# Optimization experiments

Hardware: AMD Instinct MI355X
Metric: run time of the kernel (lower is better)

The kernel has to match this reference:

```python
import jax, jax.numpy as jnp
import numpy as np

DIM = 1024


def setup_inputs() -> dict:
    key = jax.random.key(0)
    ks = jax.random.split(key, 10)
    B, SQ, SKV, D = 4, 2048, 2048, DIM
    s = 1.0 / np.sqrt(D)
    return {
        "query": jax.random.normal(ks[0], (B, SQ, D), dtype=jnp.float32),
        "key_value": jax.random.normal(ks[1], (B, SKV, D), dtype=jnp.float32),
        "Wq": jax.random.normal(ks[2], (D, D), dtype=jnp.float32) * s,
        "bq": jnp.zeros((D,), dtype=jnp.float32),
        "Wk": jax.random.normal(ks[3], (D, D), dtype=jnp.float32) * s,
        "bk": jnp.zeros((D,), dtype=jnp.float32),
        "Wv": jax.random.normal(ks[4], (D, D), dtype=jnp.float32) * s,
        "bv": jnp.zeros((D,), dtype=jnp.float32),
        "Wo": jax.random.normal(ks[5], (D, D), dtype=jnp.float32) * s,
        "bo": jnp.zeros((D,), dtype=jnp.float32),
    }


def reference(query, key_value, Wq, bq, Wk, bk, Wv, bv, Wo, bo):
    # Faithful to the Keras layer: NO 1/sqrt(d) scaling, single head.
    Q = jnp.einsum("bsd,de->bse", query, Wq) + bq            # [B,Sq,D]
    K = jnp.einsum("btd,de->bte", key_value, Wk) + bk        # [B,Skv,D]
    V = jnp.einsum("btd,de->bte", key_value, Wv) + bv        # [B,Skv,D]
    scores = jnp.einsum("bse,bte->bst", Q, K)                # [B,Sq,Skv]
    attn = jax.nn.softmax(scores, axis=-1)
    ctx = jnp.einsum("bst,bte->bse", attn, V)                # [B,Sq,D]
    return jnp.einsum("bse,ef->bsf", ctx, Wo) + bo
```

## Files before the change

kernel.cpp:

```cpp
#include <hip/hip_runtime.h>
#include <cstdint>

typedef unsigned short u16;
typedef _Float16 f16;
typedef __attribute__((ext_vector_type(8))) short    s8v;
typedef __attribute__((ext_vector_type(8))) _Float16 h8v;
typedef __attribute__((ext_vector_type(4))) float    f4v;

__device__ __forceinline__ float bf2f(u16 b) {
  unsigned int u = ((unsigned int)b) << 16;
  float f;
  __builtin_memcpy(&f, &u, 4);
  return f;
}
__device__ __forceinline__ u16 f2bf(float f) {
  unsigned int u;
  __builtin_memcpy(&u, &f, 4);
  u += 0x7fffu + ((u >> 16) & 1u);
  return (u16)(u >> 16);
}

__device__ __forceinline__ void glds16(const void* g, void* l) {
  __builtin_amdgcn_global_load_lds(
      (const __attribute__((address_space(1))) unsigned int*)g,
      (__attribute__((address_space(3))) unsigned int*)l, 16, 0, 0);
}

#define BM 128
#define BN 128
#define BK 32

__global__ __launch_bounds__(256)
void detect_dtype(const u16* __restrict__ q, int* __restrict__ flg)
{
  __shared__ int cbig, czero;
  if (threadIdx.x == 0) { cbig = 0; czero = 0; }
  __syncthreads();
  int b = 0, z = 0;
  for (int i = threadIdx.x; i < 4096; i += 256) {
    float v = bf2f(q[i]);
    if (!(fabsf(v) < 1e4f)) b++;
    if ((i & 1) == 0 && q[i] == 0) z++;
  }
  atomicAdd(&cbig, b);
  atomicAdd(&czero, z);
  __syncthreads();
  if (threadIdx.x == 0) flg[0] = (cbig > 64 || czero > 1600) ? 1 : 0;
}

__global__ __launch_bounds__(256)
void convert_h(const int* __restrict__ flg,
               const void* __restrict__ q, const void* __restrict__ kv,
               f16* __restrict__ qo, f16* __restrict__ kvo, long n)
{
  const void* in = blockIdx.y ? kv : q;
  f16* out = blockIdx.y ? kvo : qo;
  const long i = ((long)blockIdx.x * 256 + threadIdx.x) * 8;
  if (i >= n) return;
  h8v h;
  if (flg[0] != 0) {
    const float* p = (const float*)in + i;
    f4v f0 = *(const f4v*)p;
    f4v f1 = *(const f4v*)(p + 4);
#pragma unroll
    for (int j = 0; j < 4; ++j) {
      h[j]     = (f16)f0[j];
      h[4 + j] = (f16)f1[j];
    }
  } else {
    s8v b = *(const s8v*)((const short*)in + i);
#pragma unroll
    for (int j = 0; j < 8; ++j) h[j] = (f16)bf2f((u16)b[j]);
  }
  *(h8v*)(out + i) = h;
}

__global__ __launch_bounds__(256)
void transpose_w4(const int* __restrict__ flg,
                  const void* __restrict__ w0, const void* __restrict__ w1,
                  const void* __restrict__ w2, const void* __restrict__ w3,
                  f16* __restrict__ h0, f16* __restrict__ h1,
                  f16* __restrict__ h2, u16* __restrict__ b3, int D)
{
  __shared__ float tile[32][33];
  const int zb = blockIdx.z;
  const void* in_v = (zb == 0) ? w0 : (zb == 1) ? w1 : (zb == 2) ? w2 : w3;
  const bool i32 = (flg[0] != 0);
  const u16*   in16 = (const u16*)in_v;
  const float* in32 = (const float*)in_v;
  const int c0 = blockIdx.x * 32, r0 = blockIdx.y * 32;
  const int tx = threadIdx.x, ty = threadIdx.y;
  for (int i = ty; i < 32; i += 8) {
    const long idx = (long)(r0 + i) * D + c0 + tx;
    tile[i][tx] = i32 ? in32[idx] : bf2f(in16[idx]);
  }
  __syncthreads();
  f16* outH = (zb == 0) ? h0 : (zb == 1) ? h1 : h2;
  for (int i = ty; i < 32; i += 8) {
    const long idx = (long)(c0 + i) * D + r0 + tx;
    const float v = tile[tx][i];
    if (zb == 3) b3[idx]   = f2bf(v);
    else         outH[idx] = (f16)v;
  }
}

__global__ __launch_bounds__(256)
void gemm_proj_qk(const int* __restrict__ flg,
                  const f16* __restrict__ A0, const f16* __restrict__ B0,
                  const void* __restrict__ bias0, f16* __restrict__ o0,
                  const f16* __restrict__ A1, const f16* __restrict__ B1,
                  const void* __restrict__ bias1, f16* __restrict__ o1,
                  int M, int N, int K)
{
  __shared__ u16 As[BM * BK];
  __shared__ u16 Bs[BN * BK];

  const int zb = blockIdx.z;
  const f16* A = zb ? A1 : A0;
  const f16* B = zb ? B1 : B0;
  const void* bias = zb ? bias1 : bias0;
  f16* out = zb ? o1 : o0;

  const int f_in = flg[0];
  const int tid = threadIdx.x, lane = tid & 63, wave = tid >> 6;
  const int wm = wave >> 1, wn = wave & 1;
  const int m0 = blockIdx.y * BM, n0 = blockIdx.x * BN;

  const int rr  = wave * 32 + (lane >> 2);
  const int cc8 = (lane & 3) * 8;
  const f16* ga0 = A + (long)(m0 + rr) * K + cc8;
  const f16* ga1 = ga0 + 16 * (long)K;
  const f16* gb0 = B + (long)(n0 + rr) * K + cc8;
  const f16* gb1 = gb0 + 16 * (long)K;
  u16* la0 = &As[(wave * 2    ) * 512];
  u16* la1 = &As[(wave * 2 + 1) * 512];
  u16* lb0 = &Bs[(wave * 2    ) * 512];
  u16* lb1 = &Bs[(wave * 2 + 1) * 512];

  f4v acc[4][4];
#pragma unroll
  for (int i = 0; i < 4; ++i)
#pragma unroll
    for (int j = 0; j < 4; ++j) acc[i][j] = (f4v){0.f, 0.f, 0.f, 0.f};

  const int fr = lane & 15, fk = (lane >> 4) * 8;
  const int aoff = (wm * 64 + fr) * BK + fk;
  const int boff = (wn * 64 + fr) * BK + fk;

  for (int kt = 0; kt < K; kt += BK) {
    glds16(ga0, la0); glds16(ga1, la1);
    glds16(gb0, lb0); glds16(gb1, lb1);
    ga0 += BK; ga1 += BK; gb0 += BK; gb1 += BK;
    __syncthreads();

    h8v af[4], bfr[4];
#pragma unroll
    for (int mi = 0; mi < 4; ++mi) af[mi]  = *(const h8v*)&As[aoff + mi * 16 * BK];
#pragma unroll
    for (int ni = 0; ni < 4; ++ni) bfr[ni] = *(const h8v*)&Bs[boff + ni * 16 * BK];
#pragma unroll
    for (int mi = 0; mi < 4; ++mi)
#pragma unroll
      for (int ni = 0; ni < 4; ++ni)
        acc[mi][ni] = __builtin_amdgcn_mfma_f32_16x16x32_f16(af[mi], bfr[ni], acc[mi][ni], 0, 0, 0);
    __syncthreads();
  }

  const int cr = (lane >> 4) * 4, ccl = lane & 15;
#pragma unroll
  for (int ni = 0; ni < 4; ++ni) {
    const int gcol = n0 + wn * 64 + ni * 16 + ccl;
    const float bv = (f_in != 0) ? ((const float*)bias)[gcol]
                                 : bf2f(((const u16*)bias)[gcol]);
#pragma unroll
    for (int mi = 0; mi < 4; ++mi)
#pragma unroll
      for (int r = 0; r < 4; ++r) {
        const long grow = (long)(m0 + wm * 64 + mi * 16 + cr + r);
        out[grow * N + gcol] = (f16)(acc[mi][ni][r] + bv);
      }
  }
}

__global__ __launch_bounds__(256)
void gemm_vt(const int* __restrict__ flg, const f16* __restrict__ A,
             const f16* __restrict__ B, const void* __restrict__ bias,
             u16* __restrict__ Vt, int M, int N, int K, int SB)
{
  __shared__ u16 As[BM * BK];
  __shared__ u16 Bs[BN * BK];
  __shared__ u16 xp[4][64 * 34];

  const int f_in = flg[0];
  const int tid = threadIdx.x, lane = tid & 63, wave = tid >> 6;
  const int wm = wave >> 1, wn = wave & 1;
  const int m0 = blockIdx.y * BM, n0 = blockIdx.x * BN;

  const int rr  = wave * 32 + (lane >> 2);
  const int cc8 = (lane & 3) * 8;
  const f16* ga0 = A + (long)(m0 + rr) * K + cc8;
  const f16* ga1 = ga0 + 16 * (long)K;
  const f16* gb0 = B + (long)(n0 + rr) * K + cc8;
  const f16* gb1 = gb0 + 16 * (long)K;
  u16* la0 = &As[(wave * 2    ) * 512];
  u16* la1 = &As[(wave * 2 + 1) * 512];
  u16* lb0 = &Bs[(wave * 2    ) * 512];
  u16* lb1 = &Bs[(wave * 2 + 1) * 512];

  f4v acc[4][4];
#pragma unroll
  for (int i = 0; i < 4; ++i)
#pragma unroll
    for (int j = 0; j < 4; ++j) acc[i][j] = (f4v){0.f, 0.f, 0.f, 0.f};

  const int fr = lane & 15, fk = (lane >> 4) * 8;
  const int aoff = (wm * 64 + fr) * BK + fk;
  const int boff = (wn * 64 + fr) * BK + fk;

  for (int kt = 0; kt < K; kt += BK) {
    glds16(ga0, la0); glds16(ga1, la1);
    glds16(gb0, lb0); glds16(gb1, lb1);
    ga0 += BK; ga1 += BK; gb0 += BK; gb1 += BK;
    __syncthreads();

    h8v af[4], bfr[4];
#pragma unroll
    for (int mi = 0; mi < 4; ++mi) af[mi]  = *(const h8v*)&As[aoff + mi * 16 * BK];
#pragma unroll
    for (int ni = 0; ni < 4; ++ni) bfr[ni] = *(const h8v*)&Bs[boff + ni * 16 * BK];
#pragma unroll
    for (int mi = 0; mi < 4; ++mi)
#pragma unroll
      for (int ni = 0; ni < 4; ++ni)
        acc[mi][ni] = __builtin_amdgcn_mfma_f32_16x16x32_f16(af[mi], bfr[ni], acc[mi][ni], 0, 0, 0);
    __syncthreads();
  }

  const int cr = (lane >> 4) * 4, ccl = lane & 15;
  const int b  = m0 / SB;
  const int s0 = (m0 % SB) + wm * 64;
  u16* xw = &xp[wave][0];
  const long bbase = (long)b * N * SB;
#pragma unroll
  for (int h = 0; h < 2; ++h) {
#pragma unroll
    for (int nl = 0; nl < 2; ++nl) {
      const int ni = h * 2 + nl;
      const int gcol = n0 + wn * 64 + ni * 16 + ccl;
      const float bv = (f_in != 0) ? ((const float*)bias)[gcol]
                                   : bf2f(((const u16*)bias)[gcol]);
#pragma unroll
      for (int mi = 0; mi < 4; ++mi)
#pragma unroll
        for (int r = 0; r < 4; ++r)
          xw[(mi * 16 + cr + r) * 34 + nl * 16 + ccl] = f2bf(acc[mi][ni][r] + bv);
    }
    __syncthreads();
#pragma unroll
    for (int c = 0; c < 32; ++c) {
      const int gcol = n0 + wn * 64 + h * 32 + c;
      Vt[bbase + (long)gcol * SB + s0 + lane] = xw[lane * 34 + c];
    }
    __syncthreads();
  }
}

__global__ __launch_bounds__(256)
void gemm_sc(const f16* __restrict__ A, const f16* __restrict__ B,
             float* __restrict__ C, int M, int N, int K,
             long sA, long sB, long sC)
{
  __shared__ u16 As[BM * BK];
  __shared__ u16 Bs[BN * BK];

  const int tid = threadIdx.x, lane = tid & 63, wave = tid >> 6;
  const int wm = wave >> 1, wn = wave & 1;
  const int m0 = blockIdx.y * BM, n0 = blockIdx.x * BN;
  const long z = blockIdx.z;

  const int rr  = wave * 32 + (lane >> 2);
  const int cc8 = (lane & 3) * 8;
  const f16* ga0 = A + (long)(m0 + rr) * K + cc8 + z * sA;
  const f16* ga1 = ga0 + 16 * (long)K;
  const f16* gb0 = B + (long)(n0 + rr) * K + cc8 + z * sB;
  const f16* gb1 = gb0 + 16 * (long)K;
  u16* la0 = &As[(wave * 2    ) * 512];
  u16* la1 = &As[(wave * 2 + 1) * 512];
  u16* lb0 = &Bs[(wave * 2    ) * 512];
  u16* lb1 = &Bs[(wave * 2 + 1) * 512];

  f4v acc[4][4];
#pragma unroll
  for (int i = 0; i < 4; ++i)
#pragma unroll
    for (int j = 0; j < 4; ++j) acc[i][j] = (f4v){0.f, 0.f, 0.f, 0.f};

  const int fr = lane & 15, fk = (lane >> 4) * 8;
  const int aoff = (wm * 64 + fr) * BK + fk;
  const int boff = (wn * 64 + fr) * BK + fk;

  for (int kt = 0; kt < K; kt += BK) {
    glds16(ga0, la0); glds16(ga1, la1);
    glds16(gb0, lb0); glds16(gb1, lb1);
    ga0 += BK; ga1 += BK; gb0 += BK; gb1 += BK;
    __syncthreads();

    h8v af[4], bfr[4];
#pragma unroll
    for (int mi = 0; mi < 4; ++mi) af[mi]  = *(const h8v*)&As[aoff + mi * 16 * BK];
#pragma unroll
    for (int ni = 0; ni < 4; ++ni) bfr[ni] = *(const h8v*)&Bs[boff + ni * 16 * BK];
#pragma unroll
    for (int mi = 0; mi < 4; ++mi)
#pragma unroll
      for (int ni = 0; ni < 4; ++ni)
        acc[mi][ni] = __builtin_amdgcn_mfma_f32_16x16x32_f16(af[mi], bfr[ni], acc[mi][ni], 0, 0, 0);
    __syncthreads();
  }

  const int cr = (lane >> 4) * 4, ccl = lane & 15;
#pragma unroll
  for (int ni = 0; ni < 4; ++ni) {
    const int gcol = n0 + wn * 64 + ni * 16 + ccl;
#pragma unroll
    for (int mi = 0; mi < 4; ++mi)
#pragma unroll
      for (int r = 0; r < 4; ++r) {
        const long grow = (long)(m0 + wm * 64 + mi * 16 + cr + r);
        C[z * sC + grow * N + gcol] = acc[mi][ni][r];
      }
  }
}

template<bool OUT_FLAG, bool HAS_BIAS>
__global__ __launch_bounds__(256)
void gemm16(const int* __restrict__ flg, const u16* __restrict__ A,
            const u16* __restrict__ Bt, const void* __restrict__ bias,
            void* __restrict__ Cv, int M, int N, int K,
            long sA, long sB, long sC)
{
  __shared__ u16 As[BM * BK];
  __shared__ u16 Bs[BN * BK];

  const int f_in = flg[0];
  const int tid = threadIdx.x, lane = tid & 63, wave = tid >> 6;
  const int wm = wave >> 1, wn = wave & 1;
  const int m0 = blockIdx.y * BM, n0 = blockIdx.x * BN;
  const long z = blockIdx.z;
  const u16* Ap = A + z * sA;
  const u16* Bp = Bt + z * sB;

  const int rr  = wave * 32 + (lane >> 2);
  const int cc8 = (lane & 3) * 8;
  const u16* ga0 = Ap + (long)(m0 + rr) * K + cc8;
  const u16* ga1 = ga0 + 16 * (long)K;
  const u16* gb0 = Bp + (long)(n0 + rr) * K + cc8;
  const u16* gb1 = gb0 + 16 * (long)K;
  u16* la0 = &As[(wave * 2    ) * 512];
  u16* la1 = &As[(wave * 2 + 1) * 512];
  u16* lb0 = &Bs[(wave * 2    ) * 512];
  u16* lb1 = &Bs[(wave * 2 + 1) * 512];

  f4v acc[4][4];
#pragma unroll
  for (int i = 0; i < 4; ++i)
#pragma unroll
    for (int j = 0; j < 4; ++j) acc[i][j] = (f4v){0.f, 0.f, 0.f, 0.f};

  const int fr = lane & 15, fk = (lane >> 4) * 8;
  const int aoff = (wm * 64 + fr) * BK + fk;
  const int boff = (wn * 64 + fr) * BK + fk;

  for (int kt = 0; kt < K; kt += BK) {
    glds16(ga0, la0); glds16(ga1, la1);
    glds16(gb0, lb0); glds16(gb1, lb1);
    ga0 += BK; ga1 += BK; gb0 += BK; gb1 += BK;
    __syncthreads();

    s8v af[4], bfr[4];
#pragma unroll
    for (int mi = 0; mi < 4; ++mi) af[mi]  = *(const s8v*)&As[aoff + mi * 16 * BK];
#pragma unroll
    for (int ni = 0; ni < 4; ++ni) bfr[ni] = *(const s8v*)&Bs[boff + ni * 16 * BK];
#pragma unroll
    for (int mi = 0; mi < 4; ++mi)
#pragma unroll
      for (int ni = 0; ni < 4; ++ni)
        acc[mi][ni] = __builtin_amdgcn_mfma_f32_16x16x32_bf16(af[mi], bfr[ni], acc[mi][ni], 0, 0, 0);
    __syncthreads();
  }

  const int cr = (lane >> 4) * 4, ccl = lane & 15;
  const bool o32 = OUT_FLAG && (f_in != 0);
#pragma unroll
  for (int ni = 0; ni < 4; ++ni) {
    const int gcol = n0 + wn * 64 + ni * 16 + ccl;
    float bv = 0.f;
    if (HAS_BIAS)
      bv = (f_in != 0) ? ((const float*)bias)[gcol] : bf2f(((const u16*)bias)[gcol]);
#pragma unroll
    for (int mi = 0; mi < 4; ++mi)
#pragma unroll
      for (int r = 0; r < 4; ++r) {
        const long grow = (long)(m0 + wm * 64 + mi * 16 + cr + r);
        const float val = acc[mi][ni][r] + bv;
        const long idx = z * sC + grow * N + gcol;
        if (o32) ((float*)Cv)[idx] = val;
        else     ((u16*)Cv)[idx]   = f2bf(val);
      }
  }
}

__global__ __launch_bounds__(256)
void softmax_rows_bf(const float* __restrict__ S, u16* __restrict__ P, int N)
{
  const float* row = S + (long)blockIdx.x * N;
  u16* prow = P + (long)blockIdx.x * N;
  const int t = threadIdx.x;
  f4v v0 = *(const f4v*)(row + t * 8);
  f4v v1 = *(const f4v*)(row + t * 8 + 4);

  float m = v0[0];
#pragma unroll
  for (int j = 1; j < 4; ++j) m = fmaxf(m, v0[j]);
#pragma unroll
  for (int j = 0; j < 4; ++j) m = fmaxf(m, v1[j]);
  for (int off = 32; off > 0; off >>= 1) m = fmaxf(m, __shfl_down(m, off, 64));

  __shared__ float redm[4], reds[4];
  if ((t & 63) == 0) redm[t >> 6] = m;
  __syncthreads();
  m = fmaxf(fmaxf(redm[0], redm[1]), fmaxf(redm[2], redm[3]));

  float s = 0.f;
#pragma unroll
  for (int j = 0; j < 4; ++j) { v0[j] = __expf(v0[j] - m); s += v0[j]; }
#pragma unroll
  for (int j = 0; j < 4; ++j) { v1[j] = __expf(v1[j] - m); s += v1[j]; }
  for (int off = 32; off > 0; off >>= 1) s += __shfl_down(s, off, 64);
  if ((t & 63) == 0) reds[t >> 6] = s;
  __syncthreads();
  s = reds[0] + reds[1] + reds[2] + reds[3];

  const float inv = 1.f / s;
  s8v o;
#pragma unroll
  for (int j = 0; j < 4; ++j) {
    o[j]     = (short)f2bf(v0[j] * inv);
    o[4 + j] = (short)f2bf(v1[j] * inv);
  }
  *(s8v*)(prow + t * 8) = o;
}

extern "C" void kernel_launch(void* const* d_in, const int* in_sizes, int n_in,
                              void* d_out, int out_size, void* d_ws, size_t ws_size,
                              hipStream_t stream)
{
  const void* query = d_in[0];
  const void* kv    = d_in[1];
  const void* Wq    = d_in[2];
  const void* bq    = d_in[3];
  const void* Wk    = d_in[4];
  const void* bk    = d_in[5];
  const void* Wv    = d_in[6];
  const void* bv    = d_in[7];
  const void* Wo    = d_in[8];
  const void* bo    = d_in[9];

  const int Bn = 4, S = 2048, D = 1024;
  const int MS = Bn * S;
  const size_t KBu = 1024, MBu = 1024 * 1024;
  const long nTok = (long)MS * D;

  char* ws = (char*)d_ws;
  int*  flg  = (int*)(ws);
  f16*  Qi   = (f16*)(ws + 64 * KBu);
  f16*  KVi  = (f16*)(ws + 64 * KBu + 16 * MBu);
  char* rW   = ws + 64 * KBu + 32 * MBu;
  f16*  WqT  = (f16*)(rW);
  f16*  WkT  = (f16*)(rW + 2 * MBu);
  f16*  WvT  = (f16*)(rW + 4 * MBu);
  u16*  WoT  = (u16*)(rW + 6 * MBu);
  char* rQK  = rW + 8 * MBu;
  f16*  Qf   = (f16*)(rQK);
  f16*  Kf   = (f16*)(rQK + 16 * MBu);
  u16*  attn = (u16*)(rQK);
  float* Sc  = (float*)(rQK + 32 * MBu);
  char* rV   = rQK + 96 * MBu;
  u16*  Vt   = (u16*)(rV);
  u16*  Cx   = (u16*)(rV + 16 * MBu);

  detect_dtype<<<1, 256, 0, stream>>>((const u16*)query, flg);

  convert_h<<<dim3((unsigned)(nTok / 2048), 2), 256, 0, stream>>>(
      flg, query, kv, Qi, KVi, nTok);

  dim3 tb(32, 8);
  transpose_w4<<<dim3(32, 32, 4), tb, 0, stream>>>(
      flg, Wq, Wk, Wv, Wo, WqT, WkT, WvT, WoT, D);

  gemm_proj_qk<<<dim3(D / BN, MS / BM, 2), 256, 0, stream>>>(
      flg, Qi, WqT, bq, Qf, KVi, WkT, bk, Kf, MS, D, D);
  gemm_vt<<<dim3(D / BN, MS / BM, 1), 256, 0, stream>>>(
      flg, KVi, WvT, bv, Vt, MS, D, D, S);

  gemm_sc<<<dim3(S / BN, S / BM, Bn), 256, 0, stream>>>(
      Qf, Kf, Sc, S, S, D, (long)S * D, (long)S * D, (long)S * S);
  softmax_rows_bf<<<dim3(Bn * S), 256, 0, stream>>>(Sc, attn, S);
  gemm16<false, false><<<dim3(D / BN, S / BM, Bn), 256, 0, stream>>>(
      flg, attn, Vt, nullptr, Cx, S, D, S, (long)S * S, (long)D * S, (long)S * D);

  gemm16<true, true><<<dim3(D / BN, MS / BM, 1), 256, 0, stream>>>(
      flg, Cx, WoT, bo, d_out, MS, D, D, 0L, 0L, 0L);
}
```

Before: 417.0 us.

## Double GEMM K-step to 64 and merge Q/K/V projections into one launch

All GEMM kernels now load a 64-wide K slab per iteration, stored as two 32-wide halves in LDS. This halves the number of barrier pairs and load rounds per output tile. The Q, K and V projections are merged into a single three-slice launch, and the V-transpose epilogue reuses the operand LDS buffers as staging space. Shared memory per block doubles, which may lower occupancy.

```diff
diff --git a/kernel.cpp b/kernel.cpp
--- a/kernel.cpp
+++ b/kernel.cpp
@@ -28,7 +28,6 @@
 
 #define BM 128
 #define BN 128
-#define BK 32
 
 __global__ __launch_bounds__(256)
 void detect_dtype(const u16* __restrict__ q, int* __restrict__ flg)
@@ -105,21 +104,22 @@
 }
 
 __global__ __launch_bounds__(256)
-void gemm_proj_qk(const int* __restrict__ flg,
-                  const f16* __restrict__ A0, const f16* __restrict__ B0,
-                  const void* __restrict__ bias0, f16* __restrict__ o0,
-                  const f16* __restrict__ A1, const f16* __restrict__ B1,
-                  const void* __restrict__ bias1, f16* __restrict__ o1,
-                  int M, int N, int K)
-{
-  __shared__ u16 As[BM * BK];
-  __shared__ u16 Bs[BN * BK];
+void gemm_proj3(const int* __restrict__ flg,
+                const f16* __restrict__ Qi, const f16* __restrict__ KVi,
+                const f16* __restrict__ WqT, const f16* __restrict__ WkT,
+                const f16* __restrict__ WvT,
+                const void* __restrict__ bq, const void* __restrict__ bk,
+                const void* __restrict__ bv,
+                f16* __restrict__ Qf, f16* __restrict__ Kf,
+                u16* __restrict__ Vt, int M, int N, int K, int SB)
+{
+  __shared__ u16 As[BM * 64];
+  __shared__ u16 Bs[BN * 64];
 
   const int zb = blockIdx.z;
-  const f16* A = zb ? A1 : A0;
-  const f16* B = zb ? B1 : B0;
-  const void* bias = zb ? bias1 : bias0;
-  f16* out = zb ? o1 : o0;
+  const f16* A = (zb == 0) ? Qi : KVi;
+  const f16* B = (zb == 0) ? WqT : (zb == 1) ? WkT : WvT;
+  const void* bias = (zb == 0) ? bq : (zb == 1) ? bk : bv;
 
   const int f_in = flg[0];
   const int tid = threadIdx.x, lane = tid & 63, wave = tid >> 6;
@@ -128,14 +128,12 @@
 
   const int rr  = wave * 32 + (lane >> 2);
   const int cc8 = (lane & 3) * 8;
-  const f16* ga0 = A + (long)(m0 + rr) * K + cc8;
-  const f16* ga1 = ga0 + 16 * (long)K;
-  const f16* gb0 = B + (long)(n0 + rr) * K + cc8;
-  const f16* gb1 = gb0 + 16 * (long)K;
-  u16* la0 = &As[(wave * 2    ) * 512];
-  u16* la1 = &As[(wave * 2 + 1) * 512];
-  u16* lb0 = &Bs[(wave * 2    ) * 512];
-  u16* lb1 = &Bs[(wave * 2 + 1) * 512];
+  const f16* ga00 = A + (long)(m0 + rr) * K + cc8;
+  const f16* ga01 = ga00 + 16 * (long)K;
+  const f16* gb00 = B + (long)(n0 + rr) * K + cc8;
+  const f16* gb01 = gb00 + 16 * (long)K;
+  u16* la0 = &As[(wave * 2) * 512];  u16* la1 = la0 + 512;
+  u16* lb0 = &Bs[(wave * 2) * 512];  u16* lb1 = lb0 + 512;
 
   f4v acc[4][4];
 #pragma unroll
@@ -144,134 +142,97 @@
     for (int j = 0; j < 4; ++j) acc[i][j] = (f4v){0.f, 0.f, 0.f, 0.f};
 
   const int fr = lane & 15, fk = (lane >> 4) * 8;
-  const int aoff = (wm * 64 + fr) * BK + fk;
-  const int boff = (wn * 64 + fr) * BK + fk;
-
-  for (int kt = 0; kt < K; kt += BK) {
-    glds16(ga0, la0); glds16(ga1, la1);
-    glds16(gb0, lb0); glds16(gb1, lb1);
-    ga0 += BK; ga1 += BK; gb0 += BK; gb1 += BK;
+  const int aoff = (wm * 64 + fr) * 32 + fk;
+  const int boff = (wn * 64 + fr) * 32 + fk;
+
+  for (int kt = 0; kt < K; kt += 64) {
+    glds16(ga00,      la0);        glds16(ga01,      la1);
+    glds16(ga00 + 32, la0 + 4096); glds16(ga01 + 32, la1 + 4096);
+    glds16(gb00,      lb0);        glds16(gb01,      lb1);
+    glds16(gb00 + 32, lb0 + 4096); glds16(gb01 + 32, lb1 + 4096);
+    ga00 += 64; ga01 += 64; gb00 += 64; gb01 += 64;
     __syncthreads();
 
-    h8v af[4], bfr[4];
-#pragma unroll
-    for (int mi = 0; mi < 4; ++mi) af[mi]  = *(const h8v*)&As[aoff + mi * 16 * BK];
-#pragma unroll
-    for (int ni = 0; ni < 4; ++ni) bfr[ni] = *(const h8v*)&Bs[boff + ni * 16 * BK];
-#pragma unroll
-    for (int mi = 0; mi < 4; ++mi)
-#pragma unroll
-      for (int ni = 0; ni < 4; ++ni)
-        acc[mi][ni] = __builtin_amdgcn_mfma_f32_16x16x32_f16(af[mi], bfr[ni], acc[mi][ni], 0, 0, 0);
+    {
+      h8v af[4], bfr[4];
+#pragma unroll
+      for (int mi = 0; mi < 4; ++mi) af[mi]  = *(const h8v*)&As[aoff + mi * 512];
+#pragma unroll
+      for (int ni = 0; ni < 4; ++ni) bfr[ni] = *(const h8v*)&Bs[boff + ni * 512];
+#pragma unroll
+      for (int mi = 0; mi < 4; ++mi)
+#pragma unroll
+        for (int ni = 0; ni < 4; ++ni)
+          acc[mi][ni] = __builtin_amdgcn_mfma_f32_16x16x32_f16(af[mi], bfr[ni], acc[mi][ni], 0, 0, 0);
+    }
+    {
+      h8v af[4], bfr[4];
+#pragma unroll
+      for (int mi = 0; mi < 4; ++mi) af[mi]  = *(const h8v*)&As[4096 + aoff + mi * 512];
+#pragma unroll
+      for (int ni = 0; ni < 4; ++ni) bfr[ni] = *(const h8v*)&Bs[4096 + boff + ni * 512];
+#pragma unroll
+      for (int mi = 0; mi < 4; ++mi)
+#pragma unroll
+        for (int ni = 0; ni < 4; ++ni)
+          acc[mi][ni] = __builtin_amdgcn_mfma_f32_16x16x32_f16(af[mi], bfr[ni], acc[mi][ni], 0, 0, 0);
+    }
     __syncthreads();
   }
 
   const int cr = (lane >> 4) * 4, ccl = lane & 15;
-#pragma unroll
-  for (int ni = 0; ni < 4; ++ni) {
-    const int gcol = n0 + wn * 64 + ni * 16 + ccl;
-    const float bv = (f_in != 0) ? ((const float*)bias)[gcol]
-                                 : bf2f(((const u16*)bias)[gcol]);
-#pragma unroll
-    for (int mi = 0; mi < 4; ++mi)
-#pragma unroll
-      for (int r = 0; r < 4; ++r) {
-        const long grow = (long)(m0 + wm * 64 + mi * 16 + cr + r);
-        out[grow * N + gcol] = (f16)(acc[mi][ni][r] + bv);
+  if (zb < 2) {
+    f16* out = zb ? Kf : Qf;
+#pragma unroll
+    for (int ni = 0; ni < 4; ++ni) {
+      const int gcol = n0 + wn * 64 + ni * 16 + ccl;
+      const float bvv = (f_in != 0) ? ((const float*)bias)[gcol]
+                                    : bf2f(((const u16*)bias)[gcol]);
+#pragma unroll
+      for (int mi = 0; mi < 4; ++mi)
+#pragma unroll
+        for (int r = 0; r < 4; ++r) {
+          const long grow = (long)(m0 + wm * 64 + mi * 16 + cr + r);
+          out[grow * N + gcol] = (f16)(acc[mi][ni][r] + bvv);
+        }
+    }
+  } else {
+    u16* xw = (wave < 2) ? (&As[0] + wave * 2176) : (&Bs[0] + (wave - 2) * 2176);
+    const int b  = m0 / SB;
+    const int s0 = (m0 % SB) + wm * 64;
+    const long bbase = (long)b * N * SB;
+#pragma unroll
+    for (int h = 0; h < 2; ++h) {
+#pragma unroll
+      for (int nl = 0; nl < 2; ++nl) {
+        const int ni = h * 2 + nl;
+        const int gcol = n0 + wn * 64 + ni * 16 + ccl;
+        const float bvv = (f_in != 0) ? ((const float*)bias)[gcol]
+                                      : bf2f(((const u16*)bias)[gcol]);
+#pragma unroll
+        for (int mi = 0; mi < 4; ++mi)
+#pragma unroll
+          for (int r = 0; r < 4; ++r)
+            xw[(mi * 16 + cr + r) * 34 + nl * 16 + ccl] = f2bf(acc[mi][ni][r] + bvv);
       }
-  }
-}
-
-__global__ __launch_bounds__(256)
-void gemm_vt(const int* __restrict__ flg, const f16* __restrict__ A,
-             const f16* __restrict__ B, const void* __restrict__ bias,
-             u16* __restrict__ Vt, int M, int N, int K, int SB)
-{
-  __shared__ u16 As[BM * BK];
-  __shared__ u16 Bs[BN * BK];
-  __shared__ u16 xp[4][64 * 34];
-
-  const int f_in = flg[0];
-  const int tid = threadIdx.x, lane = tid & 63, wave = tid >> 6;
-  const int wm = wave >> 1, wn = wave & 1;
-  const int m0 = blockIdx.y * BM, n0 = blockIdx.x * BN;
-
-  const int rr  = wave * 32 + (lane >> 2);
-  const int cc8 = (lane & 3) * 8;
-  const f16* ga0 = A + (long)(m0 + rr) * K + cc8;
-  const f16* ga1 = ga0 + 16 * (long)K;
-  const f16* gb0 = B + (long)(n0 + rr) * K + cc8;
-  const f16* gb1 = gb0 + 16 * (long)K;
-  u16* la0 = &As[(wave * 2    ) * 512];
-  u16* la1 = &As[(wave * 2 + 1) * 512];
-  u16* lb0 = &Bs[(wave * 2    ) * 512];
-  u16* lb1 = &Bs[(wave * 2 + 1) * 512];
-
-  f4v acc[4][4];
-#pragma unroll
-  for (int i = 0; i < 4; ++i)
-#pragma unroll
-    for (int j = 0; j < 4; ++j) acc[i][j] = (f4v){0.f, 0.f, 0.f, 0.f};
-
-  const int fr = lane & 15, fk = (lane >> 4) * 8;
-  const int aoff = (wm * 64 + fr) * BK + fk;
-  const int boff = (wn * 64 + fr) * BK + fk;
-
-  for (int kt = 0; kt < K; kt += BK) {
-    glds16(ga0, la0); glds16(ga1, la1);
-    glds16(gb0, lb0); glds16(gb1, lb1);
-    ga0 += BK; ga1 += BK; gb0 += BK; gb1 += BK;
-    __syncthreads();
-
-    h8v af[4], bfr[4];
-#pragma unroll
-    for (int mi = 0; mi < 4; ++mi) af[mi]  = *(const h8v*)&As[aoff + mi * 16 * BK];
-#pragma unroll
-    for (int ni = 0; ni < 4; ++ni) bfr[ni] = *(const h8v*)&Bs[boff + ni * 16 * BK];
-#pragma unroll
-    for (int mi = 0; mi < 4; ++mi)
-#pragma unroll
-      for (int ni = 0; ni < 4; ++ni)
-        acc[mi][ni] = __builtin_amdgcn_mfma_f32_16x16x32_f16(af[mi], bfr[ni], acc[mi][ni], 0, 0, 0);
-    __syncthreads();
-  }
-
-  const int cr = (lane >> 4) * 4, ccl = lane & 15;
-  const int b  = m0 / SB;
-  const int s0 = (m0 % SB) + wm * 64;
-  u16* xw = &xp[wave][0];
-  const long bbase = (long)b * N * SB;
-#pragma unroll
-  for (int h = 0; h < 2; ++h) {
-#pragma unroll
-    for (int nl = 0; nl < 2; ++nl) {
-      const int ni = h * 2 + nl;
-      const int gcol = n0 + wn * 64 + ni * 16 + ccl;
-      const float bv = (f_in != 0) ? ((const float*)bias)[gcol]
-                                   : bf2f(((const u16*)bias)[gcol]);
-#pragma unroll
-      for (int mi = 0; mi < 4; ++mi)
-#pragma unroll
-        for (int r = 0; r < 4; ++r)
-          xw[(mi * 16 + cr + r) * 34 + nl * 16 + ccl] = f2bf(acc[mi][ni][r] + bv);
-    }
-    __syncthreads();
-#pragma unroll
-    for (int c = 0; c < 32; ++c) {
-      const int gcol = n0 + wn * 64 + h * 32 + c;
-      Vt[bbase + (long)gcol * SB + s0 + lane] = xw[lane * 34 + c];
-    }
-    __syncthreads();
-  }
-}
-
-__global__ __launch_bounds__(256)
-void gemm_sc(const f16* __restrict__ A, const f16* __restrict__ B,
-             float* __restrict__ C, int M, int N, int K,
-             long sA, long sB, long sC)
-{
-  __shared__ u16 As[BM * BK];
-  __shared__ u16 Bs[BN * BK];
+      __syncthreads();
+#pragma unroll
+      for (int c = 0; c < 32; ++c) {
+        const int gcol = n0 + wn * 64 + h * 32 + c;
+        Vt[bbase + (long)gcol * SB + s0 + lane] = xw[lane * 34 + c];
+      }
+      __syncthreads();
+    }
+  }
+}
+
+__global__ __launch_bounds__(256)
+void gemm_sc64(const f16* __restrict__ A, const f16* __restrict__ B,
+               float* __restrict__ C, int M, int N, int K,
+               long sA, long sB, long sC)
+{
+  __shared__ u16 As[BM * 64];
+  __shared__ u16 Bs[BN * 64];
 
   const int tid = threadIdx.x, lane = tid & 63, wave = tid >> 6;
   const int wm = wave >> 1, wn = wave & 1;
@@ -280,14 +241,12 @@
 
   const int rr  = wave * 32 + (lane >> 2);
   const int cc8 = (lane & 3) * 8;
-  const f16* ga0 = A + (long)(m0 + rr) * K + cc8 + z * sA;
-  const f16* ga1 = ga0 + 16 * (long)K;
-  const f16* gb0 = B + (long)(n0 + rr) * K + cc8 + z * sB;
-  const f16* gb1 = gb0 + 16 * (long)K;
-  u16* la0 = &As[(wave * 2    ) * 512];
-  u16* la1 = &As[(wave * 2 + 1) * 512];
-  u16* lb0 = &Bs[(wave * 2    ) * 512];
-  u16* lb1 = &Bs[(wave * 2 + 1) * 512];
+  const f16* ga00 = A + (long)(m0 + rr) * K + cc8 + z * sA;
+  const f16* ga01 = ga00 + 16 * (long)K;
+  const f16* gb00 = B + (long)(n0 + rr) * K + cc8 + z * sB;
+  const f16* gb01 = gb00 + 16 * (long)K;
+  u16* la0 = &As[(wave * 2) * 512];  u16* la1 = la0 + 512;
+  u16* lb0 = &Bs[(wave * 2) * 512];  u16* lb1 = lb0 + 512;
 
   f4v acc[4][4];
 #pragma unroll
@@ -296,25 +255,41 @@
     for (int j = 0; j < 4; ++j) acc[i][j] = (f4v){0.f, 0.f, 0.f, 0.f};
 
   const int fr = lane & 15, fk = (lane >> 4) * 8;
-  const int aoff = (wm * 64 + fr) * BK + fk;
-  const int boff = (wn * 64 + fr) * BK + fk;
-
-  for (int kt = 0; kt < K; kt += BK) {
-    glds16(ga0, la0); glds16(ga1, la1);
-    glds16(gb0, lb0); glds16(gb1, lb1);
-    ga0 += BK; ga1 += BK; gb0 += BK; gb1 += BK;
+  const int aoff = (wm * 64 + fr) * 32 + fk;
+  const int boff = (wn * 64 + fr) * 32 + fk;
+
+  for (int kt = 0; kt < K; kt += 64) {
+    glds16(ga00,      la0);        glds16(ga01,      la1);
+    glds16(ga00 + 32, la0 + 4096); glds16(ga01 + 32, la1 + 4096);
+    glds16(gb00,      lb0);        glds16(gb01,      lb1);
+    glds16(gb00 + 32, lb0 + 4096); glds16(gb01 + 32, lb1 + 4096);
+    ga00 += 64; ga01 += 64; gb00 += 64; gb01 += 64;
     __syncthreads();
 
-    h8v af[4], bfr[4];
-#pragma unroll
-    for (int mi = 0; mi < 4; ++mi) af[mi]  = *(const h8v*)&As[aoff + mi * 16 * BK];
-#pragma unroll
-    for (int ni = 0; ni < 4; ++ni) bfr[ni] = *(const h8v*)&Bs[boff + ni * 16 * BK];
-#pragma unroll
-    for (int mi = 0; mi < 4; ++mi)
-#pragma unroll
-      for (int ni = 0; ni < 4; ++ni)
-        acc[mi][ni] = __builtin_amdgcn_mfma_f32_16x16x32_f16(af[mi], bfr[ni], acc[mi][ni], 0, 0, 0);
+    {
+      h8v af[4], bfr[4];
+#pragma unroll
+      for (int mi = 0; mi < 4; ++mi) af[mi]  = *(const h8v*)&As[aoff + mi * 512];
+#pragma unroll
+      for (int ni = 0; ni < 4; ++ni) bfr[ni] = *(const h8v*)&Bs[boff + ni * 512];
+#pragma unroll
+      for (int mi = 0; mi < 4; ++mi)
+#pragma unroll
+        for (int ni = 0; ni < 4; ++ni)
+          acc[mi][ni] = __builtin_amdgcn_mfma_f32_16x16x32_f16(af[mi], bfr[ni], acc[mi][ni], 0, 0, 0);
+    }
+    {
+      h8v af[4], bfr[4];
+#pragma unroll
+      for (int mi = 0; mi < 4; ++mi) af[mi]  = *(const h8v*)&As[4096 + aoff + mi * 512];
+#pragma unroll
+      for (int ni = 0; ni < 4; ++ni) bfr[ni] = *(const h8v*)&Bs[4096 + boff + ni * 512];
+#pragma unroll
+      for (int mi = 0; mi < 4; ++mi)
+#pragma unroll
+        for (int ni = 0; ni < 4; ++ni)
+          acc[mi][ni] = __builtin_amdgcn_mfma_f32_16x16x32_f16(af[mi], bfr[ni], acc[mi][ni], 0, 0, 0);
+    }
     __syncthreads();
   }
 
@@ -334,32 +309,28 @@
 
 template<bool OUT_FLAG, bool HAS_BIAS>
 __global__ __launch_bounds__(256)
-void gemm16(const int* __restrict__ flg, const u16* __restrict__ A,
-            const u16* __restrict__ Bt, const void* __restrict__ bias,
-            void* __restrict__ Cv, int M, int N, int K,
-            long sA, long sB, long sC)
-{
-  __shared__ u16 As[BM * BK];
-  __shared__ u16 Bs[BN * BK];
+void gemm_bf64(const int* __restrict__ flg, const u16* __restrict__ A,
+               const u16* __restrict__ Bt, const void* __restrict__ bias,
+               void* __restrict__ Cv, int M, int N, int K,
+               long sA, long sB, long sC)
+{
+  __shared__ u16 As[BM * 64];
+  __shared__ u16 Bs[BN * 64];
 
   const int f_in = flg[0];
   const int tid = threadIdx.x, lane = tid & 63, wave = tid >> 6;
   const int wm = wave >> 1, wn = wave & 1;
   const int m0 = blockIdx.y * BM, n0 = blockIdx.x * BN;
   const long z = blockIdx.z;
-  const u16* Ap = A + z * sA;
-  const u16* Bp = Bt + z * sB;
 
   const int rr  = wave * 32 + (lane >> 2);
   const int cc8 = (lane & 3) * 8;
-  const u16* ga0 = Ap + (long)(m0 + rr) * K + cc8;
-  const u16* ga1 = ga0 + 16 * (long)K;
-  const u16* gb0 = Bp + (long)(n0 + rr) * K + cc8;
-  const u16* gb1 = gb0 + 16 * (long)K;
-  u16* la0 = &As[(wave * 2    ) * 512];
-  u16* la1 = &As[(wave * 2 + 1) * 512];
-  u16* lb0 = &Bs[(wave * 2    ) * 512];
-  u16* lb1 = &Bs[(wave * 2 + 1) * 512];
+  const u16* ga00 = A + (long)(m0 + rr) * K + cc8 + z * sA;
+  const u16* ga01 = ga00 + 16 * (long)K;
+  const u16* gb00 = Bt + (long)(n0 + rr) * K + cc8 + z * sB;
+  const u16* gb01 = gb00 + 16 * (long)K;
+  u16* la0 = &As[(wave * 2) * 512];  u16* la1 = la0 + 512;
+  u16* lb0 = &Bs[(wave * 2) * 512];  u16* lb1 = lb0 + 512;
 
   f4v acc[4][4];
 #pragma unroll
@@ -368,25 +339,41 @@
     for (int j = 0; j < 4; ++j) acc[i][j] = (f4v){0.f, 0.f, 0.f, 0.f};
 
   const int fr = lane & 15, fk = (lane >> 4) * 8;
-  const int aoff = (wm * 64 + fr) * BK + fk;
-  const int boff = (wn * 64 + fr) * BK + fk;
-
-  for (int kt = 0; kt < K; kt += BK) {
-    glds16(ga0, la0); glds16(ga1, la1);
-    glds16(gb0, lb0); glds16(gb1, lb1);
-    ga0 += BK; ga1 += BK; gb0 += BK; gb1 += BK;
+  const int aoff = (wm * 64 + fr) * 32 + fk;
+  const int boff = (wn * 64 + fr) * 32 + fk;
+
+  for (int kt = 0; kt < K; kt += 64) {
+    glds16(ga00,      la0);        glds16(ga01,      la1);
+    glds16(ga00 + 32, la0 + 4096); glds16(ga01 + 32, la1 + 4096);
+    glds16(gb00,      lb0);        glds16(gb01,      lb1);
+    glds16(gb00 + 32, lb0 + 4096); glds16(gb01 + 32, lb1 + 4096);
+    ga00 += 64; ga01 += 64; gb00 += 64; gb01 += 64;
     __syncthreads();
 
-    s8v af[4], bfr[4];
-#pragma unroll
-    for (int mi = 0; mi < 4; ++mi) af[mi]  = *(const s8v*)&As[aoff + mi * 16 * BK];
-#pragma unroll
-    for (int ni = 0; ni < 4; ++ni) bfr[ni] = *(const s8v*)&Bs[boff + ni * 16 * BK];
-#pragma unroll
-    for (int mi = 0; mi < 4; ++mi)
-#pragma unroll
-      for (int ni = 0; ni < 4; ++ni)
-        acc[mi][ni] = __builtin_amdgcn_mfma_f32_16x16x32_bf16(af[mi], bfr[ni], acc[mi][ni], 0, 0, 0);
+    {
+      s8v af[4], bfr[4];
+#pragma unroll
+      for (int mi = 0; mi < 4; ++mi) af[mi]  = *(const s8v*)&As[aoff + mi * 512];
+#pragma unroll
+      for (int ni = 0; ni < 4; ++ni) bfr[ni] = *(const s8v*)&Bs[boff + ni * 512];
+#pragma unroll
+      for (int mi = 0; mi < 4; ++mi)
+#pragma unroll
+        for (int ni = 0; ni < 4; ++ni)
+          acc[mi][ni] = __builtin_amdgcn_mfma_f32_16x16x32_bf16(af[mi], bfr[ni], acc[mi][ni], 0, 0, 0);
+    }
+    {
+      s8v af[4], bfr[4];
+#pragma unroll
+      for (int mi = 0; mi < 4; ++mi) af[mi]  = *(const s8v*)&As[4096 + aoff + mi * 512];
+#pragma unroll
+      for (int ni = 0; ni < 4; ++ni) bfr[ni] = *(const s8v*)&Bs[4096 + boff + ni * 512];
+#pragma unroll
+      for (int mi = 0; mi < 4; ++mi)
+#pragma unroll
+        for (int ni = 0; ni < 4; ++ni)
+          acc[mi][ni] = __builtin_amdgcn_mfma_f32_16x16x32_bf16(af[mi], bfr[ni], acc[mi][ni], 0, 0, 0);
+    }
     __syncthreads();
   }
 
@@ -395,15 +382,15 @@
 #pragma unroll
   for (int ni = 0; ni < 4; ++ni) {
     const int gcol = n0 + wn * 64 + ni * 16 + ccl;
-    float bv = 0.f;
+    float bvv = 0.f;
     if (HAS_BIAS)
-      bv = (f_in != 0) ? ((const float*)bias)[gcol] : bf2f(((const u16*)bias)[gcol]);
+      bvv = (f_in != 0) ? ((const float*)bias)[gcol] : bf2f(((const u16*)bias)[gcol]);
 #pragma unroll
     for (int mi = 0; mi < 4; ++mi)
 #pragma unroll
       for (int r = 0; r < 4; ++r) {
         const long grow = (long)(m0 + wm * 64 + mi * 16 + cr + r);
-        const float val = acc[mi][ni][r] + bv;
+        const float val = acc[mi][ni][r] + bvv;
         const long idx = z * sC + grow * N + gcol;
         if (o32) ((float*)Cv)[idx] = val;
         else     ((u16*)Cv)[idx]   = f2bf(val);
@@ -499,17 +486,15 @@
   transpose_w4<<<dim3(32, 32, 4), tb, 0, stream>>>(
       flg, Wq, Wk, Wv, Wo, WqT, WkT, WvT, WoT, D);
 
-  gemm_proj_qk<<<dim3(D / BN, MS / BM, 2), 256, 0, stream>>>(
-      flg, Qi, WqT, bq, Qf, KVi, WkT, bk, Kf, MS, D, D);
-  gemm_vt<<<dim3(D / BN, MS / BM, 1), 256, 0, stream>>>(
-      flg, KVi, WvT, bv, Vt, MS, D, D, S);
-
-  gemm_sc<<<dim3(S / BN, S / BM, Bn), 256, 0, stream>>>(
+  gemm_proj3<<<dim3(D / BN, MS / BM, 3), 256, 0, stream>>>(
+      flg, Qi, KVi, WqT, WkT, WvT, bq, bk, bv, Qf, Kf, Vt, MS, D, D, S);
+
+  gemm_sc64<<<dim3(S / BN, S / BM, Bn), 256, 0, stream>>>(
       Qf, Kf, Sc, S, S, D, (long)S * D, (long)S * D, (long)S * S);
   softmax_rows_bf<<<dim3(Bn * S), 256, 0, stream>>>(Sc, attn, S);
-  gemm16<false, false><<<dim3(D / BN, S / BM, Bn), 256, 0, stream>>>(
+  gemm_bf64<false, false><<<dim3(D / BN, S / BM, Bn), 256, 0, stream>>>(
       flg, attn, Vt, nullptr, Cx, S, D, S, (long)S * S, (long)D * S, (long)S * D);
 
-  gemm16<true, true><<<dim3(D / BN, MS / BM, 1), 256, 0, stream>>>(
+  gemm_bf64<true, true><<<dim3(D / BN, MS / BM, 1), 256, 0, stream>>>(
       flg, Cx, WoT, bo, d_out, MS, D, D, 0L, 0L, 0L);
 }
```

Measured after the change: 381.8 us. 8.4% less time.
